# Optimization experiments

Hardware: AMD Instinct MI355X
Metric: run time of the kernel (lower is better)

The kernel has to match this reference:

```python
import jax, jax.numpy as jnp
import numpy as np

TOPK = 2048


def setup_inputs() -> dict:
    key = jax.random.key(0)
    ks = jax.random.split(key, 16)
    M = 20000
    boxes = jax.random.uniform(ks[0], (M, 4), dtype=jnp.float32)
    scores = jax.random.uniform(ks[1], (M,), dtype=jnp.float32)
    classes = jax.random.randint(ks[2], (M,), 0, 80, dtype=jnp.int64)
    def lin(k, fan_in, fan_out):
        b = 1.0 / np.sqrt(fan_in)
        kw, kb = jax.random.split(k)
        w = jax.random.uniform(kw, (fan_in, fan_out), jnp.float32, -b, b)
        bias = jax.random.uniform(kb, (fan_out,), jnp.float32, -b, b)
        return w, bias
    sup_w1, sup_b1 = lin(ks[3], 7, 32)
    sup_w2, sup_b2 = lin(ks[4], 32, 16)
    sup_w3, sup_b3 = lin(ks[5], 16, 1)
    lam_w1, lam_b1 = lin(ks[6], 5, 16)
    lam_w2, lam_b2 = lin(ks[7], 16, 1)
    return {
        'boxes': boxes, 'scores': scores, 'classes': classes,
        'sup_w1': sup_w1, 'sup_b1': sup_b1, 'sup_w2': sup_w2, 'sup_b2': sup_b2,
        'sup_w3': sup_w3, 'sup_b3': sup_b3,
        'lam_w1': lam_w1, 'lam_b1': lam_b1, 'lam_w2': lam_w2, 'lam_b2': lam_b2,
    }


def _box_iou(b):
    # b: [N,4] in (x, y, w, h)
    x, y, w, h = b[:, 0], b[:, 1], b[:, 2], b[:, 3]
    area = w * h
    ix1 = jnp.maximum(x[:, None], x[None, :])
    iy1 = jnp.maximum(y[:, None], y[None, :])
    ix2 = jnp.minimum((x + w)[:, None], (x + w)[None, :])
    iy2 = jnp.minimum((y + h)[:, None], (y + h)[None, :])
    inter = jnp.clip(ix2 - ix1, 0) * jnp.clip(iy2 - iy1, 0)
    union = area[:, None] + area[None, :] - inter
    return inter / (union + 1e-06)


def _dacs(boxes, scores, classes,
          sup_w1, sup_b1, sup_w2, sup_b2, sup_w3, sup_b3,
          lam_w1, lam_b1, lam_w2, lam_b2):
    k = min(TOPK, scores.shape[0])
    top_scores, idx = jax.lax.top_k(scores, k)
    b = boxes[idx]            # [N,4]
    cls = classes[idx]        # [N]
    N = k
    iou = _box_iou(b)         # [N,N]
    D = iou.mean(axis=1)      # [N]
    x, y, w, h = b[:, 0], b[:, 1], b[:, 2], b[:, 3]
    feats = jnp.stack([
        iou,
        jnp.abs(x[:, None] - x[None, :]),
        jnp.abs(y[:, None] - y[None, :]),
        jnp.abs(w[:, None] - w[None, :]),
        jnp.abs(h[:, None] - h[None, :]),
        jnp.broadcast_to(top_scores[:, None], (N, N)),
        jnp.broadcast_to(top_scores[None, :], (N, N)),
    ], axis=-1)               # [N,N,7]
    hdn = jax.nn.relu(feats @ sup_w1 + sup_b1)       # [N,N,32]
    hdn = jax.nn.relu(hdn @ sup_w2 + sup_b2)         # [N,N,16]
    s_ij = jax.nn.sigmoid((hdn @ sup_w3 + sup_b3)[..., 0])  # [N,N]
    class_mask = (cls[:, None] == cls[None, :]).astype(s_ij.dtype)
    s_ij = s_ij * class_mask
    lam_in = jnp.concatenate([b, top_scores[:, None]], axis=1)  # [N,5]
    lam_h = jax.nn.relu(lam_in @ lam_w1 + lam_b1)
    lam = jax.nn.sigmoid((lam_h @ lam_w2 + lam_b2)[:, 0])       # [N]
    S = jnp.sum(s_ij * iou, axis=1)
    E = lam * S * D
    new_scores = top_scores * jnp.exp(-E)
    return b, new_scores, cls


def reference(boxes, scores, classes,
              sup_w1, sup_b1, sup_w2, sup_b2, sup_w3, sup_b3,
              lam_w1, lam_b1, lam_w2, lam_b2):
    return _dacs(boxes, scores, classes,
                 sup_w1, sup_b1, sup_w2, sup_b2, sup_w3, sup_b3,
                 lam_w1, lam_b1, lam_w2, lam_b2)
```

## Files before the change

kernel.cpp:

```cpp
#include <hip/hip_runtime.h>
#include <math.h>

#define TOPK 2048
#define NCLS 80
#define NBIN 4096
#define CMAX 2560
#define SMAX 20480
#define K1B  32
#define STN  1024
#define PTN  1024
#define CTN  256
#define CROWS 2

struct SelP {
    const float* scores; const float* boxes; const int* classes;
    int M; int K;
    float4* sel_box; float* sel_score; int* sel_cls;
};

struct PreP {
    const int* sel_cls;
    int K;
    int* cstart;
    short* clist;
};

struct CmpP {
    const float4* sel_box; const float* sel_score; const int* sel_cls;
    const int* cstart; const short* clist;
    const float* sw1; const float* sb1; const float* sw2; const float* sb2;
    const float* sw3; const float* sb3;
    const float* lw1; const float* lb1; const float* lw2; const float* lb2;
    int K;
    float* out_boxes; float* out_scores; float* out_cls;
};

__device__ __forceinline__ float iou_of(float xi, float yi, float ai,
                                        float x2i, float y2i, float4 bj) {
    float ix1 = fmaxf(xi, bj.x), iy1 = fmaxf(yi, bj.y);
    float ix2 = fminf(x2i, bj.x + bj.z), iy2 = fminf(y2i, bj.y + bj.w);
    float iw = fmaxf(ix2 - ix1, 0.0f), ih = fmaxf(iy2 - iy1, 0.0f);
    float inter = iw * ih;
    float uni = ai + bj.z * bj.w - inter;
    return inter / (uni + 1e-6f);
}

__device__ __forceinline__ int digest12(float s) {
    int v = (int)(s * 4096.0f);
    return v < 0 ? 0 : (v > NBIN - 1 ? NBIN - 1 : v);
}

__device__ __forceinline__ float key_score(unsigned long long kk) {
    unsigned mono = (unsigned)(kk >> 32);
    unsigned ob = (mono & 0x80000000u) ? (mono & 0x7FFFFFFFu) : ~mono;
    return __uint_as_float(ob);
}

__global__ __launch_bounds__(STN, 1) void k_sel(SelP p) {
    __shared__ float ssc[SMAX];
    __shared__ int   bincur[NBIN];
    __shared__ int   binbase[NBIN];
    __shared__ unsigned long long skeys[CMAX];
    __shared__ int   sfx[STN];
    __shared__ int   wsum[STN / 64];
    __shared__ int   sh_cT;

    int tid = threadIdx.x, bid = blockIdx.x;
    int M = p.M, K = p.K, M4 = M >> 2;

    for (int b = tid; b < NBIN; b += STN) bincur[b] = 0;
    __syncthreads();

    const float4* s4p = (const float4*)p.scores;
    for (int i4 = tid; i4 < M4; i4 += STN) {
        float4 v = s4p[i4];
        if (i4 < SMAX / 4) ((float4*)ssc)[i4] = v;
        atomicAdd(&bincur[digest12(v.x)], 1);
        atomicAdd(&bincur[digest12(v.y)], 1);
        atomicAdd(&bincur[digest12(v.z)], 1);
        atomicAdd(&bincur[digest12(v.w)], 1);
    }
    for (int i = M4 * 4 + tid; i < M; i += STN) {
        float s = p.scores[i];
        if (i < SMAX) ssc[i] = s;
        atomicAdd(&bincur[digest12(s)], 1);
    }
    __syncthreads();

    {
        const int BPT = NBIN / STN;
        int c0 = tid * BPT, sum = 0;
        #pragma unroll
        for (int u = 0; u < BPT; u++) sum += bincur[c0 + u];
        int lane = tid & 63;
        int x = sum;
        #pragma unroll
        for (int off = 1; off < 64; off <<= 1) {
            int v = __shfl_down(x, off, 64);
            if (lane + off < 64) x += v;
        }
        if (lane == 0) wsum[tid >> 6] = x;
        __syncthreads();
        if (tid < STN / 64) {
            int t = wsum[tid];
            #pragma unroll
            for (int off = 1; off < STN / 64; off <<= 1) {
                int v = __shfl_down(t, off, 64);
                if (tid + off < STN / 64) t += v;
            }
            wsum[tid] = t;
        }
        __syncthreads();
        int wid = tid >> 6;
        int higher = (wid < STN / 64 - 1) ? wsum[wid + 1] : 0;
        sfx[tid] = x + higher;
    }
    __syncthreads();

    {
        const int BPT = NBIN / STN;
        int running = (tid < STN - 1) ? sfx[tid + 1] : 0;
        int c0 = tid * BPT;
        for (int u = BPT - 1; u >= 0; u--) {
            int b = c0 + u, cnt = bincur[b];
            binbase[b] = running;
            if (running < K && running + cnt >= K) sh_cT = b;
            running += cnt;
        }
    }
    __syncthreads();
    int cT = sh_cT;
    for (int b = tid; b < NBIN; b += STN) bincur[b] = binbase[b];
    __syncthreads();

    for (int i = tid; i < M; i += STN) {
        float s = (i < SMAX) ? ssc[i] : p.scores[i];
        int d = digest12(s);
        if (d >= cT) {
            int slot = atomicAdd(&bincur[d], 1);
            if (slot < CMAX) {
                unsigned b = __float_as_uint(s);
                b = (b & 0x80000000u) ? ~b : (b | 0x80000000u);
                skeys[slot] = ((unsigned long long)b << 32) |
                              (unsigned long long)(0xFFFFFFFFu - (unsigned)i);
            }
        }
    }
    __syncthreads();

    {
        int C = bincur[cT]; if (C > CMAX) C = CMAX;
        const float4* boxes4 = (const float4*)p.boxes;
        for (int s = tid; s < C; s += STN) {
            unsigned long long ks = skeys[s];
            unsigned idx = 0xFFFFFFFFu - (unsigned)(ks & 0xFFFFFFFFull);
            if ((int)(idx & (K1B - 1)) != bid) continue;
            float sc = key_score(ks);
            int d = digest12(sc);
            int st = binbase[d], en = bincur[d]; if (en > CMAX) en = CMAX;
            int r = binbase[d];
            for (int t = st; t < en; t++) r += (skeys[t] > ks) ? 1 : 0;
            if (r < K) {
                p.sel_box[r] = boxes4[idx];
                p.sel_score[r] = sc;
                p.sel_cls[r] = p.classes[idx];
            }
        }
    }
}

__global__ __launch_bounds__(PTN, 1) void k_prep(PreP p) {
    __shared__ int ccnt[NCLS];
    __shared__ int ccur[NCLS];
    __shared__ int wtot;

    int tid = threadIdx.x;
    int K = p.K;
    if (tid < NCLS) ccnt[tid] = 0;
    __syncthreads();

    for (int r = tid; r < K; r += PTN) atomicAdd(&ccnt[p.sel_cls[r]], 1);
    __syncthreads();

    int x = 0, v = 0;
    if (tid < 128) {
        v = (tid < NCLS) ? ccnt[tid] : 0;
        x = v;
        #pragma unroll
        for (int off = 1; off < 64; off <<= 1) {
            int t = __shfl_up(x, off, 64);
            if ((tid & 63) >= off) x += t;
        }
        if (tid == 63) wtot = x;
    }
    __syncthreads();
    if (tid < NCLS) {
        int excl = x - v + ((tid >= 64) ? wtot : 0);
        ccur[tid] = excl;
        p.cstart[tid] = excl;
    }
    if (tid == 0) p.cstart[NCLS] = K;
    __syncthreads();

    for (int r = tid; r < K; r += PTN) {
        int pos = atomicAdd(&ccur[p.sel_cls[r]], 1);
        p.clist[pos] = (short)r;
    }
}

__global__ __launch_bounds__(CTN, 2) void k_cmp(CmpP p) {
    __shared__ float swt[914];
    __shared__ float wpart[8];
    __shared__ int   rowc[CROWS];
    __shared__ int   prefix[CROWS + 1];
    __shared__ float Ssum[CROWS], Drow[CROWS];

    int tid = threadIdx.x, bid = blockIdx.x;
    int K = p.K;
    int r0 = bid * CROWS;
    int nrows = K - r0; if (nrows > CROWS) nrows = CROWS;
    if (nrows <= 0) return;

    for (int t = tid; t < 224; t += CTN) swt[t] = p.sw1[t];
    if (tid < 32) swt[224 + tid] = p.sb1[tid];
    for (int t = tid; t < 512; t += CTN) swt[256 + t] = p.sw2[t];
    if (tid < 16) swt[768 + tid] = p.sb2[tid];
    if (tid < 16) swt[784 + tid] = p.sw3[tid];
    if (tid == 0) swt[800] = p.sb3[0];
    if (tid < 80) swt[801 + tid] = p.lw1[tid];
    if (tid < 16) swt[881 + tid] = p.lb1[tid];
    if (tid < 16) swt[897 + tid] = p.lw2[tid];
    if (tid == 0) swt[913] = p.lb2[0];

    if (tid < CROWS) {
        Ssum[tid] = 0.0f;
        int st = 0, cnt = 0;
        if (tid < nrows) {
            int c = p.sel_cls[r0 + tid];
            st = p.cstart[c];
            cnt = p.cstart[c + 1] - st;
        }
        rowc[tid] = st;
        prefix[tid] = cnt;
    }
    __syncthreads();
    if (tid == 0) {
        int a0 = prefix[0], a1 = prefix[1];
        prefix[0] = 0; prefix[1] = a0; prefix[2] = a0 + a1;
    }

    {
        float4 bi0 = p.sel_box[r0];
        float4 bi1 = (nrows > 1) ? p.sel_box[r0 + 1] : bi0;
        float a0 = bi0.z * bi0.w, x20 = bi0.x + bi0.z, y20 = bi0.y + bi0.w;
        float a1 = bi1.z * bi1.w, x21 = bi1.x + bi1.z, y21 = bi1.y + bi1.w;
        float d0 = 0.0f, d1 = 0.0f;
        for (int j = tid; j < K; j += CTN) {
            float4 bj = p.sel_box[j];
            d0 += iou_of(bi0.x, bi0.y, a0, x20, y20, bj);
            d1 += iou_of(bi1.x, bi1.y, a1, x21, y21, bj);
        }
        #pragma unroll
        for (int off = 32; off >= 1; off >>= 1) {
            d0 += __shfl_xor(d0, off, 64);
            d1 += __shfl_xor(d1, off, 64);
        }
        int lane = tid & 63, wv = tid >> 6;
        if (lane == 0) { wpart[wv * 2] = d0; wpart[wv * 2 + 1] = d1; }
    }
    __syncthreads();
    if (tid < nrows)
        Drow[tid] = (wpart[tid] + wpart[2 + tid] + wpart[4 + tid] + wpart[6 + tid])
                    / (float)K;

    int Pb = prefix[CROWS];
    const float* W1 = swt;       const float* B1 = swt + 224;
    const float* W2 = swt + 256; const float* B2 = swt + 768;
    const float* W3 = swt + 784; float B3 = swt[800];

    for (int pp = tid; pp < Pb; pp += CTN) {
        int row = (pp >= prefix[1]) ? 1 : 0;
        int j = (int)p.clist[rowc[row] + (pp - prefix[row])];
        float4 bi = p.sel_box[r0 + row];
        float4 bj = p.sel_box[j];
        float ai = bi.z * bi.w, x2i = bi.x + bi.z, y2i = bi.y + bi.w;
        float iou = iou_of(bi.x, bi.y, ai, x2i, y2i, bj);
        float f1 = fabsf(bi.x - bj.x), f2 = fabsf(bi.y - bj.y);
        float f3 = fabsf(bi.z - bj.z), f4 = fabsf(bi.w - bj.w);
        float f5 = p.sel_score[r0 + row], f6 = p.sel_score[j];
        float acc2[16];
        #pragma unroll
        for (int q = 0; q < 16; q++) acc2[q] = B2[q];
        #pragma unroll 2
        for (int o = 0; o < 32; o++) {
            float a = B1[o];
            a += iou * W1[0 * 32 + o];
            a += f1 * W1[1 * 32 + o];
            a += f2 * W1[2 * 32 + o];
            a += f3 * W1[3 * 32 + o];
            a += f4 * W1[4 * 32 + o];
            a += f5 * W1[5 * 32 + o];
            a += f6 * W1[6 * 32 + o];
            float h = fmaxf(a, 0.0f);
            #pragma unroll
            for (int q = 0; q < 16; q++) acc2[q] += h * W2[o * 16 + q];
        }
        float acc3 = B3;
        #pragma unroll
        for (int q = 0; q < 16; q++) acc3 += fmaxf(acc2[q], 0.0f) * W3[q];
        atomicAdd(&Ssum[row], iou / (1.0f + expf(-acc3)));
    }
    __syncthreads();

    if (tid < nrows) {
        int r = r0 + tid;
        float4 bi = p.sel_box[r];
        float si = p.sel_score[r];
        const float* LW1 = swt + 801; const float* LB1 = swt + 881;
        const float* LW2 = swt + 897; float LB2 = swt[913];
        float in5[5] = { bi.x, bi.y, bi.z, bi.w, si };
        float acc = LB2;
        #pragma unroll
        for (int o = 0; o < 16; o++) {
            float a2 = LB1[o];
            #pragma unroll
            for (int f = 0; f < 5; f++) a2 += in5[f] * LW1[f * 16 + o];
            acc += fmaxf(a2, 0.0f) * LW2[o];
        }
        float lam = 1.0f / (1.0f + expf(-acc));
        ((float4*)p.out_boxes)[r] = bi;
        p.out_cls[r] = (float)p.sel_cls[r];
        p.out_scores[r] = si * expf(-lam * Ssum[tid] * Drow[tid]);
    }
}

extern "C" void kernel_launch(void* const* d_in, const int* in_sizes, int n_in,
                              void* d_out, int out_size, void* d_ws, size_t ws_size,
                              hipStream_t stream) {
    int M = in_sizes[1];
    int K = (M < TOPK) ? M : TOPK;

    char* ws = (char*)d_ws;
    float4* sel_box   = (float4*)ws;           ws += (size_t)TOPK * 16;
    float*  sel_score = (float*)ws;            ws += (size_t)TOPK * 4;
    int*    sel_cls   = (int*)ws;              ws += (size_t)TOPK * 4;
    int*    cstart    = (int*)ws;              ws += (size_t)(NCLS + 2) * 4;
    short*  clist     = (short*)ws;            ws += (size_t)TOPK * 2;

    SelP sp;
    sp.scores  = (const float*)d_in[1];
    sp.boxes   = (const float*)d_in[0];
    sp.classes = (const int*)d_in[2];
    sp.M = M; sp.K = K;
    sp.sel_box = sel_box; sp.sel_score = sel_score; sp.sel_cls = sel_cls;

    PreP pp;
    pp.sel_cls = sel_cls; pp.K = K;
    pp.cstart = cstart; pp.clist = clist;

    CmpP cp;
    cp.sel_box = sel_box; cp.sel_score = sel_score; cp.sel_cls = sel_cls;
    cp.cstart = cstart; cp.clist = clist;
    cp.sw1 = (const float*)d_in[3];  cp.sb1 = (const float*)d_in[4];
    cp.sw2 = (const float*)d_in[5];  cp.sb2 = (const float*)d_in[6];
    cp.sw3 = (const float*)d_in[7];  cp.sb3 = (const float*)d_in[8];
    cp.lw1 = (const float*)d_in[9];  cp.lb1 = (const float*)d_in[10];
    cp.lw2 = (const float*)d_in[11]; cp.lb2 = (const float*)d_in[12];
    cp.K = K;
    cp.out_boxes  = (float*)d_out;
    cp.out_scores = (float*)d_out + (size_t)K * 4;
    cp.out_cls    = (float*)d_out + (size_t)K * 5;

    k_sel<<<K1B, STN, 0, stream>>>(sp);
    k_prep<<<1, PTN, 0, stream>>>(pp);
    k_cmp<<<(K + CROWS - 1) / CROWS, CTN, 0, stream>>>(cp);
}
```

Before: 106.4 us.

## Fuse class-bucketing prep kernel into top-k selection kernel and drop score LDS cache

Removes the separate single-block k_prep launch. Block 0 of k_sel now ranks every candidate, builds per-class counts, prefix offsets and the class list in shared memory. The 80KB shared score cache is removed, and the second pass re-reads scores from global memory as float4. This saves a kernel launch and a global round-trip of sel_cls, at the cost of block 0 doing all C rank computations serially, which may lengthen k_sel's critical path.

```diff
diff --git a/kernel.cpp b/kernel.cpp
--- a/kernel.cpp
+++ b/kernel.cpp
@@ -5,10 +5,8 @@
 #define NCLS 80
 #define NBIN 4096
 #define CMAX 2560
-#define SMAX 20480
 #define K1B  32
 #define STN  1024
-#define PTN  1024
 #define CTN  256
 #define CROWS 2
 
@@ -16,11 +14,6 @@
     const float* scores; const float* boxes; const int* classes;
     int M; int K;
     float4* sel_box; float* sel_score; int* sel_cls;
-};
-
-struct PreP {
-    const int* sel_cls;
-    int K;
     int* cstart;
     short* clist;
 };
@@ -57,34 +50,35 @@
 }
 
 __global__ __launch_bounds__(STN, 1) void k_sel(SelP p) {
-    __shared__ float ssc[SMAX];
     __shared__ int   bincur[NBIN];
     __shared__ int   binbase[NBIN];
     __shared__ unsigned long long skeys[CMAX];
     __shared__ int   sfx[STN];
     __shared__ int   wsum[STN / 64];
     __shared__ int   sh_cT;
+    __shared__ int   cls_of[CMAX];
+    __shared__ int   rk_of[CMAX];
+    __shared__ int   ccnt[NCLS], ccur[NCLS];
+    __shared__ int   wtot;
 
     int tid = threadIdx.x, bid = blockIdx.x;
     int M = p.M, K = p.K, M4 = M >> 2;
+    bool prep = (bid == 0);
 
     for (int b = tid; b < NBIN; b += STN) bincur[b] = 0;
+    if (tid < NCLS) ccnt[tid] = 0;
     __syncthreads();
 
     const float4* s4p = (const float4*)p.scores;
     for (int i4 = tid; i4 < M4; i4 += STN) {
         float4 v = s4p[i4];
-        if (i4 < SMAX / 4) ((float4*)ssc)[i4] = v;
         atomicAdd(&bincur[digest12(v.x)], 1);
         atomicAdd(&bincur[digest12(v.y)], 1);
         atomicAdd(&bincur[digest12(v.z)], 1);
         atomicAdd(&bincur[digest12(v.w)], 1);
     }
-    for (int i = M4 * 4 + tid; i < M; i += STN) {
-        float s = p.scores[i];
-        if (i < SMAX) ssc[i] = s;
-        atomicAdd(&bincur[digest12(s)], 1);
-    }
+    for (int i = M4 * 4 + tid; i < M; i += STN)
+        atomicAdd(&bincur[digest12(p.scores[i])], 1);
     __syncthreads();
 
     {
@@ -133,8 +127,26 @@
     for (int b = tid; b < NBIN; b += STN) bincur[b] = binbase[b];
     __syncthreads();
 
-    for (int i = tid; i < M; i += STN) {
-        float s = (i < SMAX) ? ssc[i] : p.scores[i];
+    for (int i4 = tid; i4 < M4; i4 += STN) {
+        float4 v = s4p[i4];
+        #pragma unroll
+        for (int u = 0; u < 4; u++) {
+            float s = (u == 0) ? v.x : (u == 1) ? v.y : (u == 2) ? v.z : v.w;
+            int d = digest12(s);
+            if (d >= cT) {
+                int i = i4 * 4 + u;
+                int slot = atomicAdd(&bincur[d], 1);
+                if (slot < CMAX) {
+                    unsigned b = __float_as_uint(s);
+                    b = (b & 0x80000000u) ? ~b : (b | 0x80000000u);
+                    skeys[slot] = ((unsigned long long)b << 32) |
+                                  (unsigned long long)(0xFFFFFFFFu - (unsigned)i);
+                }
+            }
+        }
+    }
+    for (int i = M4 * 4 + tid; i < M; i += STN) {
+        float s = p.scores[i];
         int d = digest12(s);
         if (d >= cT) {
             int slot = atomicAdd(&bincur[d], 1);
@@ -148,63 +160,63 @@
     }
     __syncthreads();
 
+    int C = bincur[cT]; if (C > CMAX) C = CMAX;
     {
-        int C = bincur[cT]; if (C > CMAX) C = CMAX;
         const float4* boxes4 = (const float4*)p.boxes;
         for (int s = tid; s < C; s += STN) {
             unsigned long long ks = skeys[s];
             unsigned idx = 0xFFFFFFFFu - (unsigned)(ks & 0xFFFFFFFFull);
-            if ((int)(idx & (K1B - 1)) != bid) continue;
+            bool mine = ((int)(idx & (K1B - 1)) == bid);
+            if (!prep && !mine) continue;
             float sc = key_score(ks);
             int d = digest12(sc);
             int st = binbase[d], en = bincur[d]; if (en > CMAX) en = CMAX;
             int r = binbase[d];
             for (int t = st; t < en; t++) r += (skeys[t] > ks) ? 1 : 0;
-            if (r < K) {
+            bool ok = (r < K);
+            int c = -1;
+            if (ok) c = p.classes[idx];
+            if (prep) {
+                cls_of[s] = ok ? c : -1;
+                rk_of[s] = r;
+                if (ok) atomicAdd(&ccnt[c], 1);
+            }
+            if (mine && ok) {
                 p.sel_box[r] = boxes4[idx];
                 p.sel_score[r] = sc;
-                p.sel_cls[r] = p.classes[idx];
-            }
-        }
-    }
-}
-
-__global__ __launch_bounds__(PTN, 1) void k_prep(PreP p) {
-    __shared__ int ccnt[NCLS];
-    __shared__ int ccur[NCLS];
-    __shared__ int wtot;
-
-    int tid = threadIdx.x;
-    int K = p.K;
-    if (tid < NCLS) ccnt[tid] = 0;
-    __syncthreads();
-
-    for (int r = tid; r < K; r += PTN) atomicAdd(&ccnt[p.sel_cls[r]], 1);
-    __syncthreads();
-
-    int x = 0, v = 0;
-    if (tid < 128) {
-        v = (tid < NCLS) ? ccnt[tid] : 0;
-        x = v;
-        #pragma unroll
-        for (int off = 1; off < 64; off <<= 1) {
-            int t = __shfl_up(x, off, 64);
-            if ((tid & 63) >= off) x += t;
-        }
-        if (tid == 63) wtot = x;
-    }
-    __syncthreads();
-    if (tid < NCLS) {
-        int excl = x - v + ((tid >= 64) ? wtot : 0);
-        ccur[tid] = excl;
-        p.cstart[tid] = excl;
-    }
-    if (tid == 0) p.cstart[NCLS] = K;
-    __syncthreads();
-
-    for (int r = tid; r < K; r += PTN) {
-        int pos = atomicAdd(&ccur[p.sel_cls[r]], 1);
-        p.clist[pos] = (short)r;
+                p.sel_cls[r] = c;
+            }
+        }
+    }
+    __syncthreads();
+
+    if (prep) {
+        int x = 0, v = 0;
+        if (tid < 128) {
+            v = (tid < NCLS) ? ccnt[tid] : 0;
+            x = v;
+            #pragma unroll
+            for (int off = 1; off < 64; off <<= 1) {
+                int t = __shfl_up(x, off, 64);
+                if ((tid & 63) >= off) x += t;
+            }
+            if (tid == 63) wtot = x;
+        }
+        __syncthreads();
+        if (tid < NCLS) {
+            int excl = x - v + ((tid >= 64) ? wtot : 0);
+            ccur[tid] = excl;
+            p.cstart[tid] = excl;
+        }
+        if (tid == 0) p.cstart[NCLS] = K;
+        __syncthreads();
+        for (int s = tid; s < C; s += STN) {
+            int c = cls_of[s];
+            if (c >= 0) {
+                int pos = atomicAdd(&ccur[c], 1);
+                p.clist[pos] = (short)rk_of[s];
+            }
+        }
     }
 }
 
@@ -353,10 +365,7 @@
     sp.classes = (const int*)d_in[2];
     sp.M = M; sp.K = K;
     sp.sel_box = sel_box; sp.sel_score = sel_score; sp.sel_cls = sel_cls;
-
-    PreP pp;
-    pp.sel_cls = sel_cls; pp.K = K;
-    pp.cstart = cstart; pp.clist = clist;
+    sp.cstart = cstart; sp.clist = clist;
 
     CmpP cp;
     cp.sel_box = sel_box; cp.sel_score = sel_score; cp.sel_cls = sel_cls;
@@ -372,6 +381,5 @@
     cp.out_cls    = (float*)d_out + (size_t)K * 5;
 
     k_sel<<<K1B, STN, 0, stream>>>(sp);
-    k_prep<<<1, PTN, 0, stream>>>(pp);
     k_cmp<<<(K + CROWS - 1) / CROWS, CTN, 0, stream>>>(cp);
 }
```

New measurement: 106.8 us. Within noise of the previous version (+0.3%).
